# Performance work log

Hardware: AMD Instinct MI355X
Metric: run time of the kernel (lower is better)

The kernel has to match this reference:

```python
import jax, jax.numpy as jnp
import numpy as np

F = 16      # frames
NV = 4096   # visual points per frame
NT = 512    # tactile points per frame
M = 4096    # model points
SCALE = 0.1


def setup_inputs() -> dict:
    key = jax.random.key(0)
    ks = jax.random.split(key, 6)
    return {
        "state": jax.random.normal(ks[0], (6,), dtype=jnp.float32) * 0.1,
        "model_points": jax.random.normal(ks[1], (M, 3), dtype=jnp.float32),
        "visual_points": jax.random.normal(ks[2], (F, NV, 3), dtype=jnp.float32),
        "tactile_points": jax.random.normal(ks[3], (F, NT, 3), dtype=jnp.float32),
        "physics_pred_states": jax.random.normal(ks[4], (F, 12), dtype=jnp.float32) * 0.1,
        "delta_time": jax.random.uniform(ks[5], (F,), dtype=jnp.float32, minval=0.01, maxval=0.05),
    }


def _skew(a):
    z = jnp.zeros((), a.dtype)
    return jnp.array([[z, -a[2], a[1]],
                      [a[2], z, -a[0]],
                      [-a[1], a[0], z]])


def _rot_from_omega(omega, dt):
    # Rodrigues: R = I + sin(theta*dt) S + (1 - cos(theta*dt)) S@S, S = skew(omega/|omega|)
    theta = jnp.linalg.norm(omega)
    ax = omega / jnp.clip(theta, 1e-8)
    S = _skew(ax)
    return jnp.eye(3, dtype=omega.dtype) + jnp.sin(theta * dt) * S + (1.0 - jnp.cos(theta * dt)) * (S @ S)


def _chamfer(pred, gt):
    # rows: pred [N,3], cols: gt [M,3]; row-min of squared distances, then mean
    d = (jnp.sum(pred * pred, axis=1)[:, None]
         + jnp.sum(gt * gt, axis=1)[None, :]
         - 2.0 * pred @ gt.T)
    return jnp.mean(jnp.min(d, axis=1))


def reference(state, model_points, visual_points, tactile_points, physics_pred_states, delta_time):
    t0 = state[:3]
    r0 = _rot_from_omega(state[3:], jnp.float32(1.0))  # Euler2Mat modeled as axis-angle

    def pose_step(carry, x):
        t, r = carry
        v, omega, dt = x
        t = t + v * dt
        r = _rot_from_omega(omega, dt) @ r
        return (t, r), (t, r)

    _, (ts, rs) = jax.lax.scan(
        pose_step, (t0, r0),
        (physics_pred_states[1:, 6:9], physics_pred_states[1:, 9:12], delta_time[1:]))
    ts = jnp.concatenate([t0[None], ts], axis=0)  # [F,3]
    rs = jnp.concatenate([r0[None], rs], axis=0)  # [F,3,3]

    def frame_loss(acc, x):
        t, r, vp, tp = x
        vc = ((vp - t) @ r) / SCALE
        tc = ((tp - t) @ r) / SCALE
        acc = acc + _chamfer(vc, model_points) + 0.1 * _chamfer(tc, model_points)
        return acc, None

    E_cd, _ = jax.lax.scan(frame_loss, jnp.zeros((), jnp.float32),
                           (ts, rs, visual_points, tactile_points))
    return E_cd
```

## Files before the change

kernel.cpp:

```cpp
#include <hip/hip_runtime.h>
#include <math.h>

#define F_    16
#define NV_   4096
#define NT_   512
#define M_    4096
#define PPF_  (NV_ + NT_)
#define NPTS_ (F_ * PPF_)
#define SCALE_INV 10.0f

#define TPB   256
#define PTSB  96
#define NBLK  (NPTS_ / PTSB)
#define NMG   8
#define MPG   (M_ / NMG)
#define CHM   64
#define NCH   (MPG / CHM)
#define FS    66
#define PPL   3

__device__ inline void rot_from_omega(float ox, float oy, float oz, float dt,
                                      float* R) {
    float theta = sqrtf(ox * ox + oy * oy + oz * oz);
    float inv = 1.0f / fmaxf(theta, 1e-8f);
    float ax = ox * inv, ay = oy * inv, az = oz * inv;
    float s = sinf(theta * dt);
    float c = 1.0f - cosf(theta * dt);
    R[0] = 1.0f - c * (ay * ay + az * az);
    R[1] = -s * az + c * ax * ay;
    R[2] =  s * ay + c * ax * az;
    R[3] =  s * az + c * ax * ay;
    R[4] = 1.0f - c * (ax * ax + az * az);
    R[5] = -s * ax + c * ay * az;
    R[6] = -s * ay + c * ax * az;
    R[7] =  s * ax + c * ay * az;
    R[8] = 1.0f - c * (ax * ax + ay * ay);
}

__global__ __launch_bounds__(TPB) void chamfer_one(
    const float* __restrict__ state, const float* __restrict__ model,
    const float* __restrict__ vis, const float* __restrict__ tac,
    const float* __restrict__ phys, const float* __restrict__ dts,
    float* __restrict__ out) {
    __shared__ float4 featD[2][NMG * FS];
    __shared__ float  sposes[F_ * 12];
    __shared__ float  sRs[F_ * 9];
    __shared__ float  sdt[F_ * 3];
    __shared__ float  sdm[PTSB][NMG + 1];
    __shared__ float  sw[2];

    const int t = threadIdx.x;

    if (t < F_) {
        float ox, oy, oz, dt;
        if (t == 0) { ox = state[3]; oy = state[4]; oz = state[5]; dt = 1.0f; }
        else        { ox = phys[t * 12 + 9]; oy = phys[t * 12 + 10];
                      oz = phys[t * 12 + 11]; dt = dts[t]; }
        float Rs[9];
        rot_from_omega(ox, oy, oz, dt, Rs);
        for (int j = 0; j < 9; ++j) sRs[t * 9 + j] = Rs[j];
        if (t > 0) {
            sdt[t * 3 + 0] = phys[t * 12 + 6] * dt;
            sdt[t * 3 + 1] = phys[t * 12 + 7] * dt;
            sdt[t * 3 + 2] = phys[t * 12 + 8] * dt;
        }
    }
    if (t == 0) {
        float R[9];
        for (int j = 0; j < 9; ++j) R[j] = sRs[j];
        float tr[3] = {state[0], state[1], state[2]};
        for (int i = 0; i < F_; ++i) {
            if (i > 0) {
                tr[0] += sdt[i * 3 + 0];
                tr[1] += sdt[i * 3 + 1];
                tr[2] += sdt[i * 3 + 2];
                float Rn[9];
                const float* Rsp = sRs + i * 9;
                for (int r = 0; r < 3; ++r)
                    for (int c2 = 0; c2 < 3; ++c2)
                        Rn[r * 3 + c2] = Rsp[r * 3 + 0] * R[0 + c2] +
                                         Rsp[r * 3 + 1] * R[3 + c2] +
                                         Rsp[r * 3 + 2] * R[6 + c2];
                for (int j = 0; j < 9; ++j) R[j] = Rn[j];
            }
            float* o = sposes + i * 12;
            o[0] = tr[0]; o[1] = tr[1]; o[2] = tr[2];
            for (int j = 0; j < 9; ++j) o[3 + j] = R[j] * SCALE_INV;
        }
    }

    {
        const int g = t >> 5, m = t & 31;
        int id = g * MPG + m;
        float gx = model[id * 3 + 0], gy = model[id * 3 + 1], gz = model[id * 3 + 2];
        featD[0][g * FS + m] = make_float4(-2.0f * gx, -2.0f * gy, -2.0f * gz,
                                           gx * gx + gy * gy + gz * gz);
        id += 32;
        gx = model[id * 3 + 0]; gy = model[id * 3 + 1]; gz = model[id * 3 + 2];
        featD[0][g * FS + m + 32] = make_float4(-2.0f * gx, -2.0f * gy, -2.0f * gz,
                                                gx * gx + gy * gy + gz * gz);
    }
    __syncthreads();

    const int pl = t & 31;
    const int mg = t >> 5;
    const int f = (blockIdx.x * PTSB) / PPF_;
    const int lbase = blockIdx.x * PTSB - f * PPF_;

    float c0[PPL], c1[PPL], c2[PPL], cn[PPL], dm[PPL];
    {
        const float* ps = sposes + f * 12;
#pragma unroll
        for (int k = 0; k < PPL; ++k) {
            int loc = lbase + k * 32 + pl;
            const float* p = (loc < NV_) ? (vis + ((size_t)f * NV_ + loc) * 3)
                                         : (tac + ((size_t)f * NT_ + (loc - NV_)) * 3);
            float px = p[0], py = p[1], pz = p[2];
            float d0 = px - ps[0], d1 = py - ps[1], d2 = pz - ps[2];
            const float* R = ps + 3;
            float x = d0 * R[0] + d1 * R[3] + d2 * R[6];
            float y = d0 * R[1] + d1 * R[4] + d2 * R[7];
            float z = d0 * R[2] + d1 * R[5] + d2 * R[8];
            c0[k] = x; c1[k] = y; c2[k] = z;
            cn[k] = x * x + y * y + z * z;
            dm[k] = 3.4e38f;
        }
    }

    for (int c = 0; c < NCH; ++c) {
        const int cur = c & 1;
        if (c + 1 < NCH) {
            const int g = t >> 5, m = t & 31;
            int id = g * MPG + (c + 1) * CHM + m;
            float gx = model[id * 3 + 0], gy = model[id * 3 + 1], gz = model[id * 3 + 2];
            featD[cur ^ 1][g * FS + m] = make_float4(-2.0f * gx, -2.0f * gy, -2.0f * gz,
                                                     gx * gx + gy * gy + gz * gz);
            id += 32;
            gx = model[id * 3 + 0]; gy = model[id * 3 + 1]; gz = model[id * 3 + 2];
            featD[cur ^ 1][g * FS + m + 32] = make_float4(-2.0f * gx, -2.0f * gy, -2.0f * gz,
                                                          gx * gx + gy * gy + gz * gz);
        }
        const float4* fb = &featD[cur][mg * FS];
#pragma unroll
        for (int m = 0; m < CHM; m += 2) {
            float4 ga = fb[m];
            float4 gb = fb[m + 1];
#pragma unroll
            for (int k = 0; k < PPL; ++k) {
                float da = fmaf(ga.x, c0[k], fmaf(ga.y, c1[k], fmaf(ga.z, c2[k], ga.w)));
                float db = fmaf(gb.x, c0[k], fmaf(gb.y, c1[k], fmaf(gb.z, c2[k], gb.w)));
                dm[k] = fminf(dm[k], fminf(da, db));
            }
        }
        __syncthreads();
    }

#pragma unroll
    for (int k = 0; k < PPL; ++k) sdm[k * 32 + pl][mg] = dm[k] + cn[k];
    __syncthreads();

    float v = 0.0f;
    if (t < PTSB) {
        float mn = sdm[t][0];
#pragma unroll
        for (int i = 1; i < NMG; ++i) mn = fminf(mn, sdm[t][i]);
        const int loc = lbase + t;
        const float w = (loc < NV_) ? (1.0f / NV_) : (0.1f / NT_);
        v = mn * w;
    }
    if (t < 128) {
#pragma unroll
        for (int off = 32; off > 0; off >>= 1) v += __shfl_down(v, off);
        if ((t & 63) == 0) sw[t >> 6] = v;
    }
    __syncthreads();
    if (t == 0) atomicAdd(out, sw[0] + sw[1]);
}

extern "C" void kernel_launch(void* const* d_in, const int* in_sizes, int n_in,
                              void* d_out, int out_size, void* d_ws, size_t ws_size,
                              hipStream_t stream) {
    const float* state = (const float*)d_in[0];
    const float* model = (const float*)d_in[1];
    const float* vis   = (const float*)d_in[2];
    const float* tac   = (const float*)d_in[3];
    const float* phys  = (const float*)d_in[4];
    const float* dts   = (const float*)d_in[5];
    float* out = (float*)d_out;
    (void)d_ws; (void)ws_size;

    hipMemsetAsync(out, 0, sizeof(float), stream);
    chamfer_one<<<NBLK, TPB, 0, stream>>>(state, model, vis, tac, phys, dts, out);
}
```

Measured before the change: 101.3 us.

## Retile chamfer inner loop to 12 points per thread over 32 model groups

Reorganizes the per-block work so each thread holds 12 query points in registers and scans 32-point model chunks, with the model split into 32 groups instead of 8. Each model float4 read from LDS is now reused across more points, which raises arithmetic intensity per LDS load. Query points are transformed once by 96 threads and staged through shared memory. The next chunk is now loaded from global into registers before the compute loop and written to LDS after it, hiding the load latency. Costs are more registers per thread (launch bounds now request 3 blocks), a wider 32-way final min reduction, and possible LDS bank conflicts on the strided point reads.

```diff
diff --git a/kernel.cpp b/kernel.cpp
--- a/kernel.cpp
+++ b/kernel.cpp
@@ -12,12 +12,12 @@
 #define TPB   256
 #define PTSB  96
 #define NBLK  (NPTS_ / PTSB)
-#define NMG   8
-#define MPG   (M_ / NMG)
-#define CHM   64
+#define NG    32
+#define MPG   (M_ / NG)
+#define CHM   32
 #define NCH   (MPG / CHM)
-#define FS    66
-#define PPL   3
+#define FS    33
+#define PPL   12
 
 __device__ inline void rot_from_omega(float ox, float oy, float oz, float dt,
                                       float* R) {
@@ -37,19 +37,25 @@
     R[8] = 1.0f - c * (ax * ax + ay * ay);
 }
 
-__global__ __launch_bounds__(TPB) void chamfer_one(
+__global__ __launch_bounds__(TPB, 3) void chamfer_one(
     const float* __restrict__ state, const float* __restrict__ model,
     const float* __restrict__ vis, const float* __restrict__ tac,
     const float* __restrict__ phys, const float* __restrict__ dts,
     float* __restrict__ out) {
-    __shared__ float4 featD[2][NMG * FS];
+    __shared__ float4 featD[2][NG * FS];
+    __shared__ float4 spts[8][13];
     __shared__ float  sposes[F_ * 12];
     __shared__ float  sRs[F_ * 9];
     __shared__ float  sdt[F_ * 3];
-    __shared__ float  sdm[PTSB][NMG + 1];
+    __shared__ float  sdm[PTSB][NG + 1];
     __shared__ float  sw[2];
 
-    const int t = threadIdx.x;
+    const int t  = threadIdx.x;
+    const int g  = t >> 3;
+    const int m0 = t & 7;
+    const int pl = t & 7;
+    const int f  = (blockIdx.x * PTSB) / PPF_;
+    const int lbase = blockIdx.x * PTSB - f * PPF_;
 
     if (t < F_) {
         float ox, oy, oz, dt;
@@ -89,59 +95,51 @@
         }
     }
 
-    {
-        const int g = t >> 5, m = t & 31;
-        int id = g * MPG + m;
+#pragma unroll
+    for (int j2 = 0; j2 < 4; ++j2) {
+        int id = g * MPG + m0 + 8 * j2;
         float gx = model[id * 3 + 0], gy = model[id * 3 + 1], gz = model[id * 3 + 2];
-        featD[0][g * FS + m] = make_float4(-2.0f * gx, -2.0f * gy, -2.0f * gz,
-                                           gx * gx + gy * gy + gz * gz);
-        id += 32;
-        gx = model[id * 3 + 0]; gy = model[id * 3 + 1]; gz = model[id * 3 + 2];
-        featD[0][g * FS + m + 32] = make_float4(-2.0f * gx, -2.0f * gy, -2.0f * gz,
-                                                gx * gx + gy * gy + gz * gz);
-    }
-    __syncthreads();
-
-    const int pl = t & 31;
-    const int mg = t >> 5;
-    const int f = (blockIdx.x * PTSB) / PPF_;
-    const int lbase = blockIdx.x * PTSB - f * PPF_;
+        featD[0][g * FS + m0 + 8 * j2] =
+            make_float4(-2.0f * gx, -2.0f * gy, -2.0f * gz, gx * gx + gy * gy + gz * gz);
+    }
+    __syncthreads();
+
+    if (t < PTSB) {
+        int loc = lbase + t;
+        const float* p = (loc < NV_) ? (vis + ((size_t)f * NV_ + loc) * 3)
+                                     : (tac + ((size_t)f * NT_ + (loc - NV_)) * 3);
+        float px = p[0], py = p[1], pz = p[2];
+        const float* ps = sposes + f * 12;
+        float d0 = px - ps[0], d1 = py - ps[1], d2 = pz - ps[2];
+        const float* R = ps + 3;
+        float x = d0 * R[0] + d1 * R[3] + d2 * R[6];
+        float y = d0 * R[1] + d1 * R[4] + d2 * R[7];
+        float z = d0 * R[2] + d1 * R[5] + d2 * R[8];
+        spts[t / PPL][t % PPL] = make_float4(x, y, z, x * x + y * y + z * z);
+    }
+    __syncthreads();
 
     float c0[PPL], c1[PPL], c2[PPL], cn[PPL], dm[PPL];
-    {
-        const float* ps = sposes + f * 12;
-#pragma unroll
-        for (int k = 0; k < PPL; ++k) {
-            int loc = lbase + k * 32 + pl;
-            const float* p = (loc < NV_) ? (vis + ((size_t)f * NV_ + loc) * 3)
-                                         : (tac + ((size_t)f * NT_ + (loc - NV_)) * 3);
-            float px = p[0], py = p[1], pz = p[2];
-            float d0 = px - ps[0], d1 = py - ps[1], d2 = pz - ps[2];
-            const float* R = ps + 3;
-            float x = d0 * R[0] + d1 * R[3] + d2 * R[6];
-            float y = d0 * R[1] + d1 * R[4] + d2 * R[7];
-            float z = d0 * R[2] + d1 * R[5] + d2 * R[8];
-            c0[k] = x; c1[k] = y; c2[k] = z;
-            cn[k] = x * x + y * y + z * z;
-            dm[k] = 3.4e38f;
-        }
+#pragma unroll
+    for (int k = 0; k < PPL; ++k) {
+        float4 p = spts[pl][k];
+        c0[k] = p.x; c1[k] = p.y; c2[k] = p.z; cn[k] = p.w;
+        dm[k] = 3.4e38f;
     }
 
     for (int c = 0; c < NCH; ++c) {
-        const int cur = c & 1;
+        float mx[4], my[4], mz[4];
         if (c + 1 < NCH) {
-            const int g = t >> 5, m = t & 31;
-            int id = g * MPG + (c + 1) * CHM + m;
-            float gx = model[id * 3 + 0], gy = model[id * 3 + 1], gz = model[id * 3 + 2];
-            featD[cur ^ 1][g * FS + m] = make_float4(-2.0f * gx, -2.0f * gy, -2.0f * gz,
-                                                     gx * gx + gy * gy + gz * gz);
-            id += 32;
-            gx = model[id * 3 + 0]; gy = model[id * 3 + 1]; gz = model[id * 3 + 2];
-            featD[cur ^ 1][g * FS + m + 32] = make_float4(-2.0f * gx, -2.0f * gy, -2.0f * gz,
-                                                          gx * gx + gy * gy + gz * gz);
-        }
-        const float4* fb = &featD[cur][mg * FS];
-#pragma unroll
+#pragma unroll
+            for (int j2 = 0; j2 < 4; ++j2) {
+                int id = g * MPG + (c + 1) * CHM + m0 + 8 * j2;
+                mx[j2] = model[id * 3 + 0];
+                my[j2] = model[id * 3 + 1];
+                mz[j2] = model[id * 3 + 2];
+            }
+        }
+        const float4* fb = &featD[c & 1][g * FS];
+#pragma unroll 8
         for (int m = 0; m < CHM; m += 2) {
             float4 ga = fb[m];
             float4 gb = fb[m + 1];
@@ -152,18 +150,27 @@
                 dm[k] = fminf(dm[k], fminf(da, db));
             }
         }
+        if (c + 1 < NCH) {
+#pragma unroll
+            for (int j2 = 0; j2 < 4; ++j2) {
+                featD[(c + 1) & 1][g * FS + m0 + 8 * j2] =
+                    make_float4(-2.0f * mx[j2], -2.0f * my[j2], -2.0f * mz[j2],
+                                mx[j2] * mx[j2] + my[j2] * my[j2] + mz[j2] * mz[j2]);
+            }
+        }
         __syncthreads();
     }
 
 #pragma unroll
-    for (int k = 0; k < PPL; ++k) sdm[k * 32 + pl][mg] = dm[k] + cn[k];
+    for (int k = 0; k < PPL; ++k) sdm[pl * PPL + k][g] = dm[k] + cn[k];
     __syncthreads();
 
     float v = 0.0f;
     if (t < PTSB) {
-        float mn = sdm[t][0];
-#pragma unroll
-        for (int i = 1; i < NMG; ++i) mn = fminf(mn, sdm[t][i]);
+        const float* row = sdm[t];
+        float mn = row[0];
+#pragma unroll
+        for (int i = 1; i < NG; ++i) mn = fminf(mn, row[i]);
         const int loc = lbase + t;
         const float w = (loc < NV_) ? (1.0f / NV_) : (0.1f / NT_);
         v = mn * w;
```

After: 94.56 us. 6.7% less time.
